# Kernel tuning notes

Measured on AMD Instinct MI355X. Metric: run time of the kernel, lower is better.

The kernel has to match this reference:

```python
import jax, jax.numpy as jnp
import numpy as np

N = 50000      # nodes
E = 500000     # edges
IN_FEAT = 128
OUT_FEAT = 128
R = 200        # num_relations
NB = 16        # num_bases -> 8x8 blocks
SI = IN_FEAT // NB   # submat_in = 8
SO = OUT_FEAT // NB  # submat_out = 8


def setup_inputs() -> dict:
    key = jax.random.key(0)
    k1, k2, k3, k4, k5, k6, k7 = jax.random.split(key, 7)
    h = jax.random.normal(k1, (N, IN_FEAT), dtype=jnp.float32)
    norm = jax.random.uniform(k2, (N, 1), dtype=jnp.float32)
    weight = jax.random.normal(k3, (R, NB * SI * SO), dtype=jnp.float32) * 0.1
    loop_weight = jax.random.normal(k4, (IN_FEAT, OUT_FEAT), dtype=jnp.float32) * 0.1
    src = jax.random.randint(k5, (E,), 0, N, dtype=jnp.int32)
    dst = jax.random.randint(k6, (E,), 0, N, dtype=jnp.int32)
    etype = jax.random.randint(k7, (E,), 0, R, dtype=jnp.int32)
    return {"h": h, "norm": norm, "weight": weight, "loop_weight": loop_weight,
            "src": src, "dst": dst, "etype": etype}


def reference(h, norm, weight, loop_weight, src, dst, etype):
    # self-loop message: [N, out_feat]
    loop_message = h @ loop_weight
    # per-edge relation-weight gather: [E, NB, SI, SO]
    w_e = weight[etype].reshape(-1, NB, SI, SO)
    # src features as per-basis blocks: [E, NB, SI]
    x_e = h[src].reshape(-1, NB, SI)
    # block-diagonal bmm -> messages [E, out_feat]
    msg = jnp.einsum('ebi,ebio->ebo', x_e, w_e).reshape(-1, OUT_FEAT)
    # scatter-sum to destination nodes (fn.sum(msg -> h))
    agg = jax.ops.segment_sum(msg, dst, num_segments=N)
    # apply_func: multiply by per-node norm, then add self-loop and activation
    nodes = agg * norm
    nodes = nodes + loop_message
    return jax.nn.relu(nodes)
```

## Files before the change

kernel.cpp:

```cpp
#include <hip/hip_runtime.h>
#include <hip/hip_bf16.h>


#define IN_FEAT 128
#define OUT_FEAT 128
#define SCAN_CHUNK 512

__device__ inline float blo(unsigned u) { return __uint_as_float(u << 16); }
__device__ inline float bhi(unsigned u) { return __uint_as_float(u & 0xffff0000u); }
__device__ inline unsigned short f2bf(float f) {
  __hip_bfloat16 b = __float2bfloat16(f);
  return *reinterpret_cast<unsigned short*>(&b);
}

__global__ __launch_bounds__(256) void selfloop_gemm(
    const float* __restrict__ h, const float* __restrict__ lw,
    float* __restrict__ out, int n) {
  __shared__ float slw[IN_FEAT * OUT_FEAT];
  __shared__ float sh[32 * IN_FEAT];

  {
    const float4* s4 = (const float4*)lw;
    float4* d4 = (float4*)slw;
    for (int i = threadIdx.x; i < IN_FEAT * OUT_FEAT / 4; i += 256) d4[i] = s4[i];
  }

  const int cg = threadIdx.x & 31;
  const int rg = threadIdx.x >> 5;

  for (int base = blockIdx.x * 32; base < n; base += gridDim.x * 32) {
    const int nrows = min(32, n - base);
    __syncthreads();
    {
      const float4* hs = (const float4*)(h + (size_t)base * IN_FEAT);
      float4* sd = (float4*)sh;
      const int cnt = nrows * (IN_FEAT / 4);
      for (int i = threadIdx.x; i < cnt; i += 256) sd[i] = hs[i];
    }
    __syncthreads();

    float4 acc[4];
    #pragma unroll
    for (int j = 0; j < 4; ++j) acc[j] = make_float4(0.f, 0.f, 0.f, 0.f);

    #pragma unroll 4
    for (int k = 0; k < IN_FEAT; ++k) {
      const float4 w = ((const float4*)slw)[k * 32 + cg];
      #pragma unroll
      for (int j = 0; j < 4; ++j) {
        const float hv = sh[(rg + 8 * j) * IN_FEAT + k];
        acc[j].x += hv * w.x;
        acc[j].y += hv * w.y;
        acc[j].z += hv * w.z;
        acc[j].w += hv * w.w;
      }
    }

    #pragma unroll
    for (int j = 0; j < 4; ++j) {
      const int r = rg + 8 * j;
      if (r < nrows) {
        ((float4*)(out + (size_t)(base + r) * OUT_FEAT))[cg] = acc[j];
      }
    }
  }
}

__global__ __launch_bounds__(256) void k_wpack(
    const float* __restrict__ w, unsigned short* __restrict__ w16, int total) {
  const int idx = blockIdx.x * blockDim.x + threadIdx.x;
  if (idx >= total) return;
  const int r = idx >> 10;
  const int rem = idx & 1023;
  const int b = rem >> 6;
  const int q = rem & 63;
  const int opp = q >> 4;
  const int t = q & 15;
  const int i = t >> 1;
  const int j = t & 1;
  w16[idx] = f2bf(w[((size_t)r << 10) + b * 64 + i * 8 + opp * 2 + j]);
}

__global__ __launch_bounds__(256) void k_hpack(
    const float* __restrict__ h, unsigned* __restrict__ h16p, int total8) {
  const int t = blockIdx.x * blockDim.x + threadIdx.x;
  if (t >= total8) return;
  const float4 a = ((const float4*)h)[2 * t];
  const float4 b = ((const float4*)h)[2 * t + 1];
  uint4 o;
  o.x = (unsigned)f2bf(a.x) | ((unsigned)f2bf(a.y) << 16);
  o.y = (unsigned)f2bf(a.z) | ((unsigned)f2bf(a.w) << 16);
  o.z = (unsigned)f2bf(b.x) | ((unsigned)f2bf(b.y) << 16);
  o.w = (unsigned)f2bf(b.z) | ((unsigned)f2bf(b.w) << 16);
  ((uint4*)h16p)[t] = o;
}

__global__ __launch_bounds__(256) void k_hist(
    const int* __restrict__ dst, int* __restrict__ cnt, int E) {
  const int e = blockIdx.x * blockDim.x + threadIdx.x;
  if (e < E) atomicAdd(&cnt[dst[e]], 1);
}

__global__ __launch_bounds__(256) void k_chunksum(
    const int* __restrict__ cnt, int* __restrict__ bsum, int N) {
  __shared__ int s[256];
  const int t = threadIdx.x;
  const int base = blockIdx.x * SCAN_CHUNK;
  int v = 0;
  int i0 = base + t, i1 = base + 256 + t;
  if (i0 < N) v += cnt[i0];
  if (i1 < N) v += cnt[i1];
  s[t] = v;
  __syncthreads();
  for (int d = 128; d > 0; d >>= 1) {
    if (t < d) s[t] += s[t + d];
    __syncthreads();
  }
  if (t == 0) bsum[blockIdx.x] = s[0];
}

__global__ void k_scanb(int* __restrict__ bsum, int nblk) {
  const int lane = threadIdx.x;
  if (nblk <= 128) {
    int o0 = (lane < nblk) ? bsum[lane] : 0;
    int o1 = (64 + lane < nblk) ? bsum[64 + lane] : 0;
    int v0 = o0, v1 = o1;
    #pragma unroll
    for (int d = 1; d < 64; d <<= 1) {
      int t0 = __shfl_up(v0, d);
      int t1 = __shfl_up(v1, d);
      if (lane >= d) { v0 += t0; v1 += t1; }
    }
    const int total0 = __shfl(v0, 63);
    if (lane < nblk) bsum[lane] = v0 - o0;
    if (64 + lane < nblk) bsum[64 + lane] = total0 + v1 - o1;
  } else if (lane == 0) {
    int run = 0;
    for (int b = 0; b < nblk; ++b) { int v = bsum[b]; bsum[b] = run; run += v; }
  }
}

__global__ __launch_bounds__(256) void k_offsets(
    const int* __restrict__ cnt, const int* __restrict__ bsum,
    int* __restrict__ pos, int N) {
  __shared__ int s[256];
  const int t = threadIdx.x;
  const int base = blockIdx.x * SCAN_CHUNK;
  const int i0 = base + 2 * t;
  const int i1 = i0 + 1;
  const int c0 = (i0 < N) ? cnt[i0] : 0;
  const int c1 = (i1 < N) ? cnt[i1] : 0;
  const int pair = c0 + c1;
  s[t] = pair;
  __syncthreads();
  #pragma unroll
  for (int d = 1; d < 256; d <<= 1) {
    int v = (t >= d) ? s[t - d] : 0;
    __syncthreads();
    s[t] += v;
    __syncthreads();
  }
  const int ex = s[t] - pair + bsum[blockIdx.x];
  if (i0 < N) pos[i0] = ex;
  if (i1 < N) pos[i1] = ex + c0;
}

__global__ __launch_bounds__(256) void k_scatter(
    const int* __restrict__ src, const int* __restrict__ dst,
    const int* __restrict__ etype, int* __restrict__ pos,
    int2* __restrict__ srcet, int E) {
  const int e = blockIdx.x * blockDim.x + threadIdx.x;
  if (e < E) {
    const int p = atomicAdd(&pos[dst[e]], 1);
    srcet[p] = make_int2(src[e], etype[e]);
  }
}

__global__ __launch_bounds__(256) void agg_bf16(
    const unsigned short* __restrict__ h16, const float* __restrict__ norm,
    const unsigned short* __restrict__ w16, const int* __restrict__ pos,
    const int* __restrict__ cnt, const int2* __restrict__ srcet,
    float* __restrict__ out, int N) {
  const int node = (int)((blockIdx.x * blockDim.x + threadIdx.x) >> 6);
  const int lane = threadIdx.x & 63;
  if (node >= N) return;

  const int b = lane >> 2;
  const int opp = lane & 3;
  const int woff = b * 64 + opp * 16;
  const int hoff = b * 8;

  const int num = cnt[node];
  const int end = pos[node];
  const int begin = end - num;

  float a0 = 0.f, a1 = 0.f;

  for (int base = 0; base < num; base += 64) {
    const int cn = min(64, num - base);
    const int2 my = srcet[begin + base + min(lane, cn - 1)];
    #pragma unroll 4
    for (int i = 0; i < cn; ++i) {
      const int s = __shfl(my.x, i);
      const int r = __shfl(my.y, i);
      const unsigned short* wp = w16 + ((size_t)r << 10) + woff;
      const uint4 wa = *(const uint4*)(wp);
      const uint4 wb = *(const uint4*)(wp + 8);
      const uint4 xv = *(const uint4*)(h16 + ((size_t)s << 7) + hoff);

      a0 += blo(xv.x) * blo(wa.x); a1 += blo(xv.x) * bhi(wa.x);
      a0 += bhi(xv.x) * blo(wa.y); a1 += bhi(xv.x) * bhi(wa.y);
      a0 += blo(xv.y) * blo(wa.z); a1 += blo(xv.y) * bhi(wa.z);
      a0 += bhi(xv.y) * blo(wa.w); a1 += bhi(xv.y) * bhi(wa.w);
      a0 += blo(xv.z) * blo(wb.x); a1 += blo(xv.z) * bhi(wb.x);
      a0 += bhi(xv.z) * blo(wb.y); a1 += bhi(xv.z) * bhi(wb.y);
      a0 += blo(xv.w) * blo(wb.z); a1 += blo(xv.w) * bhi(wb.z);
      a0 += bhi(xv.w) * blo(wb.w); a1 += bhi(xv.w) * bhi(wb.w);
    }
  }

  const float nm = norm[node];
  const int o = b * 8 + opp * 2;
  float* outp = out + ((size_t)node << 7) + o;
  float2 prev = *(const float2*)outp;
  float2 res;
  res.x = fmaxf(prev.x + a0 * nm, 0.f);
  res.y = fmaxf(prev.y + a1 * nm, 0.f);
  *(float2*)outp = res;
}

__global__ __launch_bounds__(256) void agg(
    const float* __restrict__ h, const float* __restrict__ norm,
    const float* __restrict__ weight, const int* __restrict__ pos,
    const int* __restrict__ cnt, const int2* __restrict__ srcet,
    float* __restrict__ out, int N) {
  const int node = (int)((blockIdx.x * blockDim.x + threadIdx.x) >> 6);
  const int lane = threadIdx.x & 63;
  if (node >= N) return;

  const int b = lane >> 2;
  const int op = (lane & 3) * 2;
  const int boff = b * 64 + op;

  const int num = cnt[node];
  const int end = pos[node];
  const int begin = end - num;

  float a0 = 0.f, a1 = 0.f;

  for (int base = 0; base < num; base += 64) {
    const int cn = min(64, num - base);
    const int2 my = srcet[begin + base + min(lane, cn - 1)];
    #pragma unroll 2
    for (int i = 0; i < cn; ++i) {
      const int s = __shfl(my.x, i);
      const int r = __shfl(my.y, i);
      const float* xp = h + ((size_t)s << 7) + b * 8;
      const float4 x0 = ((const float4*)xp)[0];
      const float4 x1 = ((const float4*)xp)[1];
      const float* wp = weight + ((size_t)r << 10) + boff;
      const float2 w0 = *(const float2*)(wp);
      const float2 w1 = *(const float2*)(wp + 8);
      const float2 w2 = *(const float2*)(wp + 16);
      const float2 w3 = *(const float2*)(wp + 24);
      const float2 w4 = *(const float2*)(wp + 32);
      const float2 w5 = *(const float2*)(wp + 40);
      const float2 w6 = *(const float2*)(wp + 48);
      const float2 w7 = *(const float2*)(wp + 56);
      a0 += x0.x * w0.x; a1 += x0.x * w0.y;
      a0 += x0.y * w1.x; a1 += x0.y * w1.y;
      a0 += x0.z * w2.x; a1 += x0.z * w2.y;
      a0 += x0.w * w3.x; a1 += x0.w * w3.y;
      a0 += x1.x * w4.x; a1 += x1.x * w4.y;
      a0 += x1.y * w5.x; a1 += x1.y * w5.y;
      a0 += x1.z * w6.x; a1 += x1.z * w6.y;
      a0 += x1.w * w7.x; a1 += x1.w * w7.y;
    }
  }

  const float nm = norm[node];
  const int o = b * 8 + op;
  float* outp = out + ((size_t)node << 7) + o;
  float2 prev = *(const float2*)outp;
  float2 res;
  res.x = fmaxf(prev.x + a0 * nm, 0.f);
  res.y = fmaxf(prev.y + a1 * nm, 0.f);
  *(float2*)outp = res;
}

__global__ __launch_bounds__(256) void edge_msg(
    const float* __restrict__ h, const float* __restrict__ norm,
    const float* __restrict__ weight, const int* __restrict__ src,
    const int* __restrict__ dst, const int* __restrict__ etype,
    float* out, int E) {
  const int wave = (int)((blockIdx.x * blockDim.x + threadIdx.x) >> 6);
  const int lane = threadIdx.x & 63;
  if (wave >= E) return;

  const int s = src[wave];
  const int d = dst[wave];
  const int r = etype[wave];
  const float nrm = norm[d];

  const int b = lane >> 2;
  const int op = (lane & 3) * 2;

  const float* xp = h + (size_t)s * IN_FEAT + b * 8;
  const float4 x0 = ((const float4*)xp)[0];
  const float4 x1 = ((const float4*)xp)[1];
  float x[8] = {x0.x, x0.y, x0.z, x0.w, x1.x, x1.y, x1.z, x1.w};

  const float* wp = weight + (size_t)r * 1024 + b * 64 + op;
  float a0 = 0.f, a1 = 0.f;
  #pragma unroll
  for (int i = 0; i < 8; ++i) {
    const float2 w = *(const float2*)(wp + i * 8);
    a0 += x[i] * w.x;
    a1 += x[i] * w.y;
  }

  const int o = b * 8 + op;
  float* outp = out + (size_t)d * OUT_FEAT + o;
  atomicAdd(outp, a0 * nrm);
  atomicAdd(outp + 1, a1 * nrm);
}

__global__ __launch_bounds__(256) void relu_k(float* __restrict__ out, int n4) {
  const int i = blockIdx.x * blockDim.x + threadIdx.x;
  if (i < n4) {
    float4 v = ((const float4*)out)[i];
    v.x = fmaxf(v.x, 0.f);
    v.y = fmaxf(v.y, 0.f);
    v.z = fmaxf(v.z, 0.f);
    v.w = fmaxf(v.w, 0.f);
    ((float4*)out)[i] = v;
  }
}

extern "C" void kernel_launch(void* const* d_in, const int* in_sizes, int n_in,
                              void* d_out, int out_size, void* d_ws, size_t ws_size,
                              hipStream_t stream) {
  const float* h    = (const float*)d_in[0];
  const float* norm = (const float*)d_in[1];
  const float* w    = (const float*)d_in[2];
  const float* lw   = (const float*)d_in[3];
  const int* src    = (const int*)d_in[4];
  const int* dst    = (const int*)d_in[5];
  const int* etype  = (const int*)d_in[6];
  float* out = (float*)d_out;

  const int N = in_sizes[1];
  const int E = in_sizes[4];
  const int R = in_sizes[2] / 1024;
  const int nblk = (N + SCAN_CHUNK - 1) / SCAN_CHUNK;

  const size_t nb_bsum = (size_t)((nblk < 128) ? 128 : nblk);
  const size_t off_cnt  = (size_t)E * 8;
  const size_t off_pos  = off_cnt + (size_t)N * 4;
  const size_t off_bsum = off_pos + (size_t)N * 4;
  size_t off_h16 = off_bsum + nb_bsum * 4;
  off_h16 = (off_h16 + 15) & ~(size_t)15;
  const size_t off_w16 = off_h16 + (size_t)N * IN_FEAT * 2;
  const size_t need_full = off_w16 + (size_t)R * 1024 * 2;
  const size_t need_sort = off_bsum + nb_bsum * 4;

  selfloop_gemm<<<512, 256, 0, stream>>>(h, lw, out, N);

  if (ws_size >= need_sort) {
    char* wsb = (char*)d_ws;
    int2* srcet = (int2*)wsb;
    int* cnt  = (int*)(wsb + off_cnt);
    int* pos  = (int*)(wsb + off_pos);
    int* bsum = (int*)(wsb + off_bsum);

    const bool full = (ws_size >= need_full);
    if (full) {
      unsigned short* w16 = (unsigned short*)(wsb + off_w16);
      unsigned* h16p = (unsigned*)(wsb + off_h16);
      k_wpack<<<(R * 1024 + 255) / 256, 256, 0, stream>>>(w, w16, R * 1024);
      k_hpack<<<(N * IN_FEAT / 8 + 255) / 256, 256, 0, stream>>>(
          h, h16p, N * IN_FEAT / 8);
    }

    hipMemsetAsync(cnt, 0, (size_t)N * 4, stream);
    k_hist<<<(E + 255) / 256, 256, 0, stream>>>(dst, cnt, E);
    k_chunksum<<<nblk, 256, 0, stream>>>(cnt, bsum, N);
    k_scanb<<<1, 64, 0, stream>>>(bsum, nblk);
    k_offsets<<<nblk, 256, 0, stream>>>(cnt, bsum, pos, N);
    k_scatter<<<(E + 255) / 256, 256, 0, stream>>>(src, dst, etype, pos, srcet, E);

    if (full) {
      const unsigned short* h16 = (const unsigned short*)(wsb + off_h16);
      const unsigned short* w16 = (const unsigned short*)(wsb + off_w16);
      agg_bf16<<<(N + 3) / 4, 256, 0, stream>>>(h16, norm, w16, pos, cnt, srcet,
                                                out, N);
    } else {
      agg<<<(N + 3) / 4, 256, 0, stream>>>(h, norm, w, pos, cnt, srcet, out, N);
    }
  } else {
    edge_msg<<<(E + 3) / 4, 256, 0, stream>>>(h, norm, w, src, dst, etype, out, E);
    const int n4 = N * OUT_FEAT / 4;
    relu_k<<<(n4 + 255) / 256, 256, 0, stream>>>(out, n4);
  }
}
```

Baseline: 163.7 us.

## Use MFMA bf16 self-loop GEMM, fuse prep kernels, use fdot2 in aggregation

```diff
diff --git a/kernel.cpp b/kernel.cpp
--- a/kernel.cpp
+++ b/kernel.cpp
@@ -5,6 +5,9 @@
 #define IN_FEAT 128
 #define OUT_FEAT 128
 #define SCAN_CHUNK 512
+
+using short8  = __attribute__((ext_vector_type(8))) short;
+using float4v = __attribute__((ext_vector_type(4))) float;
 
 __device__ inline float blo(unsigned u) { return __uint_as_float(u << 16); }
 __device__ inline float bhi(unsigned u) { return __uint_as_float(u & 0xffff0000u); }
@@ -13,86 +16,98 @@
   return *reinterpret_cast<unsigned short*>(&b);
 }
 
-__global__ __launch_bounds__(256) void selfloop_gemm(
-    const float* __restrict__ h, const float* __restrict__ lw,
-    float* __restrict__ out, int n) {
-  __shared__ float slw[IN_FEAT * OUT_FEAT];
-  __shared__ float sh[32 * IN_FEAT];
-
-  {
-    const float4* s4 = (const float4*)lw;
-    float4* d4 = (float4*)slw;
-    for (int i = threadIdx.x; i < IN_FEAT * OUT_FEAT / 4; i += 256) d4[i] = s4[i];
-  }
-
-  const int cg = threadIdx.x & 31;
-  const int rg = threadIdx.x >> 5;
-
-  for (int base = blockIdx.x * 32; base < n; base += gridDim.x * 32) {
-    const int nrows = min(32, n - base);
-    __syncthreads();
-    {
-      const float4* hs = (const float4*)(h + (size_t)base * IN_FEAT);
-      float4* sd = (float4*)sh;
-      const int cnt = nrows * (IN_FEAT / 4);
-      for (int i = threadIdx.x; i < cnt; i += 256) sd[i] = hs[i];
-    }
-    __syncthreads();
-
-    float4 acc[4];
+__device__ inline float dot2bf(unsigned x, unsigned w, float c) {
+#if __has_builtin(__builtin_amdgcn_fdot2_f32_bf16)
+  typedef __bf16 bf16x2 __attribute__((ext_vector_type(2)));
+  return __builtin_amdgcn_fdot2_f32_bf16(__builtin_bit_cast(bf16x2, x),
+                                         __builtin_bit_cast(bf16x2, w), c, false);
+#else
+  return c + blo(x) * blo(w) + bhi(x) * bhi(w);
+#endif
+}
+
+__global__ __launch_bounds__(256) void k_prep(
+    const float* __restrict__ w, unsigned short* __restrict__ w16, int wtotal,
+    const float* __restrict__ h, uint4* __restrict__ h16p, int htotal8,
+    const float* __restrict__ lw, unsigned short* __restrict__ lwT,
+    const int* __restrict__ dst, int* __restrict__ cnt, int E,
+    int bw, int bh, int blw) {
+  const int bid = blockIdx.x;
+  if (bid < bw) {
+    const int idx = bid * 256 + threadIdx.x;
+    if (idx < wtotal) {
+      const int r = idx >> 10;
+      const int rem = idx & 1023;
+      const int b = rem >> 6;
+      const int q = rem & 63;
+      const int opp = q >> 4;
+      const int t = q & 15;
+      const int j = t >> 3;
+      const int i = t & 7;
+      w16[idx] = f2bf(w[((size_t)r << 10) + b * 64 + i * 8 + opp * 2 + j]);
+    }
+  } else if (bid < bw + bh) {
+    const int t = (bid - bw) * 256 + threadIdx.x;
+    if (t < htotal8) {
+      const float4 a = ((const float4*)h)[2 * t];
+      const float4 b = ((const float4*)h)[2 * t + 1];
+      uint4 o;
+      o.x = (unsigned)f2bf(a.x) | ((unsigned)f2bf(a.y) << 16);
+      o.y = (unsigned)f2bf(a.z) | ((unsigned)f2bf(a.w) << 16);
+      o.z = (unsigned)f2bf(b.x) | ((unsigned)f2bf(b.y) << 16);
+      o.w = (unsigned)f2bf(b.z) | ((unsigned)f2bf(b.w) << 16);
+      h16p[t] = o;
+    }
+  } else if (bid < bw + bh + blw) {
+    const int idx = (bid - bw - bh) * 256 + threadIdx.x;
+    if (idx < IN_FEAT * OUT_FEAT) {
+      const int o = idx >> 7;
+      const int k = idx & 127;
+      lwT[idx] = f2bf(lw[k * 128 + o]);
+    }
+  } else {
+    const int e = (bid - bw - bh - blw) * 256 + threadIdx.x;
+    if (e < E) atomicAdd(&cnt[dst[e]], 1);
+  }
+}
+
+__global__ __launch_bounds__(256) void gemm_mfma(
+    const unsigned short* __restrict__ h16, const unsigned short* __restrict__ lwT,
+    float* __restrict__ out, int N) {
+  const int wid = threadIdx.x >> 6;
+  const int lane = threadIdx.x & 63;
+  const int row0 = blockIdx.x * 64 + wid * 16;
+  if (row0 >= N) return;
+  const int m = lane & 15;
+  const int kg = (lane >> 4) * 8;
+  const int arow = min(row0 + m, N - 1);
+
+  float4v acc[8];
+  #pragma unroll
+  for (int nt = 0; nt < 8; ++nt) acc[nt] = (float4v){0.f, 0.f, 0.f, 0.f};
+
+  const unsigned short* ap = h16 + (size_t)arow * 128 + kg;
+  const unsigned short* bp = lwT + (size_t)m * 128 + kg;
+
+  #pragma unroll
+  for (int kc = 0; kc < 4; ++kc) {
+    const short8 a = *(const short8*)(ap + kc * 32);
     #pragma unroll
-    for (int j = 0; j < 4; ++j) acc[j] = make_float4(0.f, 0.f, 0.f, 0.f);
-
-    #pragma unroll 4
-    for (int k = 0; k < IN_FEAT; ++k) {
-      const float4 w = ((const float4*)slw)[k * 32 + cg];
-      #pragma unroll
-      for (int j = 0; j < 4; ++j) {
-        const float hv = sh[(rg + 8 * j) * IN_FEAT + k];
-        acc[j].x += hv * w.x;
-        acc[j].y += hv * w.y;
-        acc[j].z += hv * w.z;
-        acc[j].w += hv * w.w;
-      }
-    }
-
+    for (int nt = 0; nt < 8; ++nt) {
+      const short8 b = *(const short8*)(bp + nt * 2048 + kc * 32);
+      acc[nt] = __builtin_amdgcn_mfma_f32_16x16x32_bf16(a, b, acc[nt], 0, 0, 0);
+    }
+  }
+
+  const int crow = row0 + (lane >> 4) * 4;
+  #pragma unroll
+  for (int nt = 0; nt < 8; ++nt) {
     #pragma unroll
-    for (int j = 0; j < 4; ++j) {
-      const int r = rg + 8 * j;
-      if (r < nrows) {
-        ((float4*)(out + (size_t)(base + r) * OUT_FEAT))[cg] = acc[j];
-      }
-    }
-  }
-}
-
-__global__ __launch_bounds__(256) void k_wpack(
-    const float* __restrict__ w, unsigned short* __restrict__ w16, int total) {
-  const int idx = blockIdx.x * blockDim.x + threadIdx.x;
-  if (idx >= total) return;
-  const int r = idx >> 10;
-  const int rem = idx & 1023;
-  const int b = rem >> 6;
-  const int q = rem & 63;
-  const int opp = q >> 4;
-  const int t = q & 15;
-  const int i = t >> 1;
-  const int j = t & 1;
-  w16[idx] = f2bf(w[((size_t)r << 10) + b * 64 + i * 8 + opp * 2 + j]);
-}
-
-__global__ __launch_bounds__(256) void k_hpack(
-    const float* __restrict__ h, unsigned* __restrict__ h16p, int total8) {
-  const int t = blockIdx.x * blockDim.x + threadIdx.x;
-  if (t >= total8) return;
-  const float4 a = ((const float4*)h)[2 * t];
-  const float4 b = ((const float4*)h)[2 * t + 1];
-  uint4 o;
-  o.x = (unsigned)f2bf(a.x) | ((unsigned)f2bf(a.y) << 16);
-  o.y = (unsigned)f2bf(a.z) | ((unsigned)f2bf(a.w) << 16);
-  o.z = (unsigned)f2bf(b.x) | ((unsigned)f2bf(b.y) << 16);
-  o.w = (unsigned)f2bf(b.z) | ((unsigned)f2bf(b.w) << 16);
-  ((uint4*)h16p)[t] = o;
+    for (int r = 0; r < 4; ++r) {
+      const int row = crow + r;
+      if (row < N) out[(size_t)row * 128 + nt * 16 + m] = acc[nt][r];
+    }
+  }
 }
 
 __global__ __launch_bounds__(256) void k_hist(
@@ -208,14 +223,14 @@
       const uint4 wb = *(const uint4*)(wp + 8);
       const uint4 xv = *(const uint4*)(h16 + ((size_t)s << 7) + hoff);
 
-      a0 += blo(xv.x) * blo(wa.x); a1 += blo(xv.x) * bhi(wa.x);
-      a0 += bhi(xv.x) * blo(wa.y); a1 += bhi(xv.x) * bhi(wa.y);
-      a0 += blo(xv.y) * blo(wa.z); a1 += blo(xv.y) * bhi(wa.z);
-      a0 += bhi(xv.y) * blo(wa.w); a1 += bhi(xv.y) * bhi(wa.w);
-      a0 += blo(xv.z) * blo(wb.x); a1 += blo(xv.z) * bhi(wb.x);
-      a0 += bhi(xv.z) * blo(wb.y); a1 += bhi(xv.z) * bhi(wb.y);
-      a0 += blo(xv.w) * blo(wb.z); a1 += blo(xv.w) * bhi(wb.z);
-      a0 += bhi(xv.w) * blo(wb.w); a1 += bhi(xv.w) * bhi(wb.w);
+      a0 = dot2bf(xv.x, wa.x, a0);
+      a0 = dot2bf(xv.y, wa.y, a0);
+      a0 = dot2bf(xv.z, wa.z, a0);
+      a0 = dot2bf(xv.w, wa.w, a0);
+      a1 = dot2bf(xv.x, wb.x, a1);
+      a1 = dot2bf(xv.y, wb.y, a1);
+      a1 = dot2bf(xv.z, wb.z, a1);
+      a1 = dot2bf(xv.w, wb.w, a1);
     }
   }
 
@@ -227,6 +242,59 @@
   res.x = fmaxf(prev.x + a0 * nm, 0.f);
   res.y = fmaxf(prev.y + a1 * nm, 0.f);
   *(float2*)outp = res;
+}
+
+__global__ __launch_bounds__(256) void selfloop_gemm(
+    const float* __restrict__ h, const float* __restrict__ lw,
+    float* __restrict__ out, int n) {
+  __shared__ float slw[IN_FEAT * OUT_FEAT];
+  __shared__ float sh[32 * IN_FEAT];
+
+  {
+    const float4* s4 = (const float4*)lw;
+    float4* d4 = (float4*)slw;
+    for (int i = threadIdx.x; i < IN_FEAT * OUT_FEAT / 4; i += 256) d4[i] = s4[i];
+  }
+
+  const int cg = threadIdx.x & 31;
+  const int rg = threadIdx.x >> 5;
+
+  for (int base = blockIdx.x * 32; base < n; base += gridDim.x * 32) {
+    const int nrows = min(32, n - base);
+    __syncthreads();
+    {
+      const float4* hs = (const float4*)(h + (size_t)base * IN_FEAT);
+      float4* sd = (float4*)sh;
+      const int cnt = nrows * (IN_FEAT / 4);
+      for (int i = threadIdx.x; i < cnt; i += 256) sd[i] = hs[i];
+    }
+    __syncthreads();
+
+    float4 acc[4];
+    #pragma unroll
+    for (int j = 0; j < 4; ++j) acc[j] = make_float4(0.f, 0.f, 0.f, 0.f);
+
+    #pragma unroll 4
+    for (int k = 0; k < IN_FEAT; ++k) {
+      const float4 w = ((const float4*)slw)[k * 32 + cg];
+      #pragma unroll
+      for (int j = 0; j < 4; ++j) {
+        const float hv = sh[(rg + 8 * j) * IN_FEAT + k];
+        acc[j].x += hv * w.x;
+        acc[j].y += hv * w.y;
+        acc[j].z += hv * w.z;
+        acc[j].w += hv * w.w;
+      }
+    }
+
+    #pragma unroll
+    for (int j = 0; j < 4; ++j) {
+      const int r = rg + 8 * j;
+      if (r < nrows) {
+        ((float4*)(out + (size_t)(base + r) * OUT_FEAT))[cg] = acc[j];
+      }
+    }
+  }
 }
 
 __global__ __launch_bounds__(256) void agg(
@@ -361,43 +429,58 @@
   size_t off_h16 = off_bsum + nb_bsum * 4;
   off_h16 = (off_h16 + 15) & ~(size_t)15;
   const size_t off_w16 = off_h16 + (size_t)N * IN_FEAT * 2;
-  const size_t need_full = off_w16 + (size_t)R * 1024 * 2;
+  const size_t off_lwT = off_w16 + (size_t)R * 1024 * 2;
+  const size_t need_full = off_lwT + (size_t)IN_FEAT * OUT_FEAT * 2;
   const size_t need_sort = off_bsum + nb_bsum * 4;
 
-  selfloop_gemm<<<512, 256, 0, stream>>>(h, lw, out, N);
-
-  if (ws_size >= need_sort) {
+  if (ws_size >= need_full) {
     char* wsb = (char*)d_ws;
     int2* srcet = (int2*)wsb;
     int* cnt  = (int*)(wsb + off_cnt);
     int* pos  = (int*)(wsb + off_pos);
     int* bsum = (int*)(wsb + off_bsum);
-
-    const bool full = (ws_size >= need_full);
-    if (full) {
-      unsigned short* w16 = (unsigned short*)(wsb + off_w16);
-      unsigned* h16p = (unsigned*)(wsb + off_h16);
-      k_wpack<<<(R * 1024 + 255) / 256, 256, 0, stream>>>(w, w16, R * 1024);
-      k_hpack<<<(N * IN_FEAT / 8 + 255) / 256, 256, 0, stream>>>(
-          h, h16p, N * IN_FEAT / 8);
-    }
-
+    unsigned short* h16 = (unsigned short*)(wsb + off_h16);
+    unsigned short* w16 = (unsigned short*)(wsb + off_w16);
+    unsigned short* lwT = (unsigned short*)(wsb + off_lwT);
+
+    hipMemsetAsync(cnt, 0, (size_t)N * 4, stream);
+
+    const int wtotal = R * 1024;
+    const int htotal8 = N * IN_FEAT / 8;
+    const int bw  = (wtotal + 255) / 256;
+    const int bh  = (htotal8 + 255) / 256;
+    const int blw = (IN_FEAT * OUT_FEAT + 255) / 256;
+    const int bhist = (E + 255) / 256;
+    k_prep<<<bw + bh + blw + bhist, 256, 0, stream>>>(
+        w, w16, wtotal, h, (uint4*)h16, htotal8, lw, lwT, dst, cnt, E,
+        bw, bh, blw);
+
+    gemm_mfma<<<(N + 63) / 64, 256, 0, stream>>>(h16, lwT, out, N);
+
+    k_chunksum<<<nblk, 256, 0, stream>>>(cnt, bsum, N);
+    k_scanb<<<1, 64, 0, stream>>>(bsum, nblk);
+    k_offsets<<<nblk, 256, 0, stream>>>(cnt, bsum, pos, N);
+    k_scatter<<<(E + 255) / 256, 256, 0, stream>>>(src, dst, etype, pos, srcet, E);
+
+    agg_bf16<<<(N + 3) / 4, 256, 0, stream>>>(h16, norm, w16, pos, cnt, srcet,
+                                              out, N);
+  } else if (ws_size >= need_sort) {
+    char* wsb = (char*)d_ws;
+    int2* srcet = (int2*)wsb;
+    int* cnt  = (int*)(wsb + off_cnt);
+    int* pos  = (int*)(wsb + off_pos);
+    int* bsum = (int*)(wsb + off_bsum);
+
+    selfloop_gemm<<<512, 256, 0, stream>>>(h, lw, out, N);
     hipMemsetAsync(cnt, 0, (size_t)N * 4, stream);
     k_hist<<<(E + 255) / 256, 256, 0, stream>>>(dst, cnt, E);
     k_chunksum<<<nblk, 256, 0, stream>>>(cnt, bsum, N);
     k_scanb<<<1, 64, 0, stream>>>(bsum, nblk);
     k_offsets<<<nblk, 256, 0, stream>>>(cnt, bsum, pos, N);
     k_scatter<<<(E + 255) / 256, 256, 0, stream>>>(src, dst, etype, pos, srcet, E);
-
-    if (full) {
-      const unsigned short* h16 = (const unsigned short*)(wsb + off_h16);
-      const unsigned short* w16 = (const unsigned short*)(wsb + off_w16);
-      agg_bf16<<<(N + 3) / 4, 256, 0, stream>>>(h16, norm, w16, pos, cnt, srcet,
-                                                out, N);
-    } else {
-      agg<<<(N + 3) / 4, 256, 0, stream>>>(h, norm, w, pos, cnt, srcet, out, N);
-    }
+    agg<<<(N + 3) / 4, 256, 0, stream>>>(h, norm, w, pos, cnt, srcet, out, N);
   } else {
+    selfloop_gemm<<<512, 256, 0, stream>>>(h, lw, out, N);
     edge_msg<<<(E + 3) / 4, 256, 0, stream>>>(h, norm, w, src, dst, etype, out, E);
     const int n4 = N * OUT_FEAT / 4;
     relu_k<<<(n4 + 255) / 256, 256, 0, stream>>>(out, n4);
```

Result: faster. 152.1 us (-7.0%).
